# Performance work log

Measured on AMD Instinct MI355X. Metric: run time of the kernel, lower is better.

Reference implementation:

```python
import jax, jax.numpy as jnp
import numpy as np

L_MAX = 3
C = 512  # channels per degree


def _triples(l_max):
    ts = []
    for l1 in range(l_max + 1):
        for l2 in range(l1, l_max + 1):
            for L in range(l2 - l1, min(l_max, l1 + l2) + 1):
                ts.append((l1, l2, L))
    return ts


def setup_inputs() -> dict:
    key = jax.random.key(0)
    keys = jax.random.split(key, 4 + len(_triples(L_MAX)))
    inp = {}
    ki = 0
    for l in range(L_MAX + 1):
        inp[f"x{l}"] = jax.random.normal(keys[ki], (C, 2 * l + 1), dtype=jnp.float32)
        ki += 1
    for (l1, l2, L) in _triples(L_MAX):
        # cg[L, l2, l1] has shape [2L+1, 2l2+1, 2l1+1]
        inp[f"cg_{L}_{l2}_{l1}"] = 0.1 * jax.random.normal(
            keys[ki], (2 * L + 1, 2 * l2 + 1, 2 * l1 + 1), dtype=jnp.float32)
        ki += 1
    return inp


def reference(x0, x1, x2, x3,
              cg_0_0_0, cg_1_1_0, cg_2_2_0, cg_3_3_0,
              cg_0_1_1, cg_1_1_1, cg_2_1_1, cg_1_2_1, cg_2_2_1, cg_3_2_1,
              cg_2_3_1, cg_3_3_1,
              cg_0_2_2, cg_1_2_2, cg_2_2_2, cg_3_2_2, cg_1_3_2, cg_2_3_2,
              cg_3_3_2,
              cg_0_3_3, cg_1_3_3, cg_2_3_3, cg_3_3_3):
    xs = [x0, x1, x2, x3]
    cg_list = [cg_0_0_0, cg_1_1_0, cg_2_2_0, cg_3_3_0,
               cg_0_1_1, cg_1_1_1, cg_2_1_1, cg_1_2_1, cg_2_2_1, cg_3_2_1,
               cg_2_3_1, cg_3_3_1,
               cg_0_2_2, cg_1_2_2, cg_2_2_2, cg_3_2_2, cg_1_3_2, cg_2_3_2,
               cg_3_3_2,
               cg_0_3_3, cg_1_3_3, cg_2_3_3, cg_3_3_3]
    cg = dict(zip(_triples(L_MAX), cg_list))
    out = {L: [] for L in range(L_MAX + 1)}
    for (l1, l2, L) in _triples(L_MAX):
        # product: [i, j, 2L+1]
        p = jnp.einsum('Mnm,im,jn->ijM', cg[(l1, l2, L)], xs[l1], xs[l2])
        out[L].append(p.reshape(-1, 2 * L + 1))
    return tuple(jnp.concatenate(out[L], axis=0) for L in range(L_MAX + 1))
```

## Files before the change

kernel.cpp:

```cpp
#include <hip/hip_runtime.h>


#define C2 (512 * 512)

struct Ptrs {
    const float* x[4];
    const float* cg[23];
};

#define TRIPLE_LIST(F) \
    F(0, 0, 0, 0, 0) \
    F(1, 0, 1, 1, 4) \
    F(2, 0, 2, 2, 22) \
    F(3, 0, 3, 3, 57) \
    F(4, 1, 1, 0, 1) \
    F(5, 1, 1, 1, 7) \
    F(6, 1, 1, 2, 27) \
    F(7, 1, 2, 1, 10) \
    F(8, 1, 2, 2, 32) \
    F(9, 1, 2, 3, 64) \
    F(10, 1, 3, 2, 37) \
    F(11, 1, 3, 3, 71) \
    F(12, 2, 2, 0, 2) \
    F(13, 2, 2, 1, 13) \
    F(14, 2, 2, 2, 42) \
    F(15, 2, 2, 3, 78) \
    F(16, 2, 3, 1, 16) \
    F(17, 2, 3, 2, 47) \
    F(18, 2, 3, 3, 85) \
    F(19, 3, 3, 0, 3) \
    F(20, 3, 3, 1, 19) \
    F(21, 3, 3, 2, 52) \
    F(22, 3, 3, 3, 92)

template <int T, int L1, int L2, int LL, int OB>
__device__ __forceinline__ void triple_block(
        const Ptrs& p, float* __restrict__ out, int i, int tid,
        float* __restrict__ xT, float* __restrict__ ys, float* __restrict__ stg) {
    constexpr int NI = 2 * L1 + 1;
    constexpr int NJ = 2 * L2 + 1;
    constexpr int NW = 2 * LL + 1;

    {
        const float4* src4 = (const float4*)p.x[L2];
        float4* dst4 = (float4*)xT;
        #pragma unroll
        for (int k = tid; k < 128 * NJ; k += 256) dst4[k] = src4[k];
    }

    if (tid < NJ * NW) {
        const int n = tid / NW;
        const int M = tid % NW;
        const float* cg = p.cg[T] + (M * NJ + n) * NI;
        const float* xi = p.x[L1] + i * NI;
        float s = 0.f;
        #pragma unroll
        for (int m = 0; m < NI; ++m) s = fmaf(cg[m], xi[m], s);
        ys[tid] = s;
    }
    __syncthreads();

    float xj0[NJ], xj1[NJ];
    #pragma unroll
    for (int n = 0; n < NJ; ++n) {
        xj0[n] = xT[tid * NJ + n];
        xj1[n] = xT[(tid + 256) * NJ + n];
    }
    #pragma unroll
    for (int M = 0; M < NW; ++M) {
        float a0 = 0.f, a1 = 0.f;
        #pragma unroll
        for (int n = 0; n < NJ; ++n) {
            const float yv = ys[n * NW + M];
            a0 = fmaf(xj0[n], yv, a0);
            a1 = fmaf(xj1[n], yv, a1);
        }
        stg[tid * NW + M] = a0;
        stg[(tid + 256) * NW + M] = a1;
    }
    __syncthreads();

    const float4* s4 = (const float4*)stg;
    float4* dst = (float4*)(out + (size_t)OB * C2 + (size_t)i * (512 * NW));
    #pragma unroll
    for (int k = tid; k < 128 * NW; k += 256) dst[k] = s4[k];
}

__global__ __launch_bounds__(256) void cg_tp_kernel(Ptrs p, float* __restrict__ out) {
    __shared__ float xT[512 * 7];
    __shared__ float ys[7 * 7];
    __shared__ float stg[512 * 7];
    const int tid = threadIdx.x;
    const int t = blockIdx.x >> 9;
    const int i = blockIdx.x & 511;
    switch (t) {
#define TCASE(T, L1, L2, LL, OB) \
        case T: triple_block<T, L1, L2, LL, OB>(p, out, i, tid, xT, ys, stg); break;
        TRIPLE_LIST(TCASE)
#undef TCASE
    }
}

extern "C" void kernel_launch(void* const* d_in, const int* in_sizes, int n_in,
                              void* d_out, int out_size, void* d_ws, size_t ws_size,
                              hipStream_t stream) {
    Ptrs p;
    for (int l = 0; l < 4; ++l) p.x[l] = (const float*)d_in[l];
    for (int t = 0; t < 23; ++t) p.cg[t] = (const float*)d_in[4 + t];
    cg_tp_kernel<<<dim3(23 * 512), dim3(256), 0, stream>>>(p, (float*)d_out);
}
```

Measured before the change: 178.2 us.

## Switch to persistent wave-level work items with register-held projections

Replaces one-block-per-(triple,i) with a persistent grid in which each 64-lane wave handles half a row (256 j values) as an independent item. The per-i projection coefficients are broadcast via shuffles into registers instead of through shared memory. x[L2] is read directly from global/cache rather than staged in LDS. Block-wide barriers are replaced by per-wave LDS waitcnt fences. This aims to remove block-level synchronization, launch overhead and shared staging of inputs. In exchange it adds uncoalesced strided global loads of x rows and a larger register footprint.

After: 173.9 us. 2.4% less time.

```diff
diff --git a/kernel.cpp b/kernel.cpp
--- a/kernel.cpp
+++ b/kernel.cpp
@@ -2,6 +2,9 @@
 
 
 #define C2 (512 * 512)
+#define NBLOCKS 1472
+#define NWAVES (NBLOCKS * 4)
+#define NITEMS (23 * 512 * 2)
 
 struct Ptrs {
     const float* x[4];
@@ -33,71 +36,83 @@
     F(21, 3, 3, 2, 52) \
     F(22, 3, 3, 3, 92)
 
+__device__ __forceinline__ void lds_fence() {
+    asm volatile("s_waitcnt lgkmcnt(0)" ::: "memory");
+    __builtin_amdgcn_sched_barrier(0);
+}
+
 template <int T, int L1, int L2, int LL, int OB>
-__device__ __forceinline__ void triple_block(
-        const Ptrs& p, float* __restrict__ out, int i, int tid,
-        float* __restrict__ xT, float* __restrict__ ys, float* __restrict__ stg) {
+__device__ __forceinline__ void do_item(const Ptrs& p, float* __restrict__ out,
+                                        int i, int jh, int lane, float* stg) {
     constexpr int NI = 2 * L1 + 1;
     constexpr int NJ = 2 * L2 + 1;
     constexpr int NW = 2 * LL + 1;
+    constexpr int NY = NJ * NW;
 
+    float yr[NY];
     {
-        const float4* src4 = (const float4*)p.x[L2];
-        float4* dst4 = (float4*)xT;
-        #pragma unroll
-        for (int k = tid; k < 128 * NJ; k += 256) dst4[k] = src4[k];
-    }
-
-    if (tid < NJ * NW) {
-        const int n = tid / NW;
-        const int M = tid % NW;
+        const int lidx = (lane < NY) ? lane : 0;
+        const int n = lidx / NW;
+        const int M = lidx % NW;
         const float* cg = p.cg[T] + (M * NJ + n) * NI;
         const float* xi = p.x[L1] + i * NI;
         float s = 0.f;
         #pragma unroll
         for (int m = 0; m < NI; ++m) s = fmaf(cg[m], xi[m], s);
-        ys[tid] = s;
+        #pragma unroll
+        for (int q = 0; q < NY; ++q) yr[q] = __shfl(s, q);
     }
-    __syncthreads();
 
-    float xj0[NJ], xj1[NJ];
+    const float* xq = p.x[L2] + (jh * 256) * NJ;
+    float* ob = out + (size_t)OB * C2 + (size_t)i * (512 * NW) + jh * (256 * NW);
+
     #pragma unroll
-    for (int n = 0; n < NJ; ++n) {
-        xj0[n] = xT[tid * NJ + n];
-        xj1[n] = xT[(tid + 256) * NJ + n];
-    }
-    #pragma unroll
-    for (int M = 0; M < NW; ++M) {
-        float a0 = 0.f, a1 = 0.f;
+    for (int r4 = 0; r4 < 4; ++r4) {
+        const int row = r4 * 64 + lane;
+        const float* xrow = xq + row * NJ;
+        float xj[NJ];
+        #pragma unroll
+        for (int n = 0; n < NJ; ++n) xj[n] = xrow[n];
+
+        float acc[NW] = {};
         #pragma unroll
         for (int n = 0; n < NJ; ++n) {
-            const float yv = ys[n * NW + M];
-            a0 = fmaf(xj0[n], yv, a0);
-            a1 = fmaf(xj1[n], yv, a1);
+            #pragma unroll
+            for (int M = 0; M < NW; ++M)
+                acc[M] = fmaf(yr[n * NW + M], xj[n], acc[M]);
         }
-        stg[tid * NW + M] = a0;
-        stg[(tid + 256) * NW + M] = a1;
+        #pragma unroll
+        for (int M = 0; M < NW; ++M) stg[row * NW + M] = acc[M];
     }
-    __syncthreads();
 
-    const float4* s4 = (const float4*)stg;
-    float4* dst = (float4*)(out + (size_t)OB * C2 + (size_t)i * (512 * NW));
-    #pragma unroll
-    for (int k = tid; k < 128 * NW; k += 256) dst[k] = s4[k];
+    lds_fence();
+
+    {
+        const float4* s4 = (const float4*)stg;
+        float4* d4 = (float4*)ob;
+        #pragma unroll
+        for (int k = lane; k < 64 * NW; k += 64) d4[k] = s4[k];
+    }
+
+    lds_fence();
 }
 
 __global__ __launch_bounds__(256) void cg_tp_kernel(Ptrs p, float* __restrict__ out) {
-    __shared__ float xT[512 * 7];
-    __shared__ float ys[7 * 7];
-    __shared__ float stg[512 * 7];
-    const int tid = threadIdx.x;
-    const int t = blockIdx.x >> 9;
-    const int i = blockIdx.x & 511;
-    switch (t) {
-#define TCASE(T, L1, L2, LL, OB) \
-        case T: triple_block<T, L1, L2, LL, OB>(p, out, i, tid, xT, ys, stg); break;
-        TRIPLE_LIST(TCASE)
-#undef TCASE
+    __shared__ float stg_s[4][256 * 7];
+    const int wid = threadIdx.x >> 6;
+    const int lane = threadIdx.x & 63;
+    float* stg = stg_s[wid];
+
+    for (int item = blockIdx.x * 4 + wid; item < NITEMS; item += NWAVES) {
+        const int t = item >> 10;
+        const int i = (item >> 1) & 511;
+        const int jh = item & 1;
+        switch (t) {
+#define TC(T, L1, L2, LL, OB) \
+            case T: do_item<T, L1, L2, LL, OB>(p, out, i, jh, lane, stg); break;
+            TRIPLE_LIST(TC)
+#undef TC
+        }
     }
 }
 
@@ -107,5 +122,5 @@
     Ptrs p;
     for (int l = 0; l < 4; ++l) p.x[l] = (const float*)d_in[l];
     for (int t = 0; t < 23; ++t) p.cg[t] = (const float*)d_in[4 + t];
-    cg_tp_kernel<<<dim3(23 * 512), dim3(256), 0, stream>>>(p, (float*)d_out);
+    cg_tp_kernel<<<dim3(NBLOCKS), dim3(256), 0, stream>>>(p, (float*)d_out);
 }
```
